# Kernel tuning notes

Measured on AMD Instinct MI355X. Metric: run time of the kernel, lower is better.

The kernel has to match this reference:

```python
import jax, jax.numpy as jnp
from jax import lax
import numpy as np

B, FRAMES, H, W = 8, 128, 64, 64
N_MFCC = 60
VID_FEAT = 196
D = VID_FEAT + N_MFCC   # COMBINE_SIZE = 256
ED = 2 * D              # mamba d_inner = 512
NST = 16                # d_state
DTR = 16                # dt_rank = ceil(D/16)
NL = 4                  # layers per direction
NC = 2                  # num_classes


def setup_inputs() -> dict:
    key = jax.random.key(0)
    ks = iter(jax.random.split(key, 64))
    def rn(shape, s=0.02):
        return jax.random.normal(next(ks), shape, jnp.float32) * s
    inp = {
        'video_input': jax.random.normal(next(ks), (B, FRAMES, 3, H, W), jnp.float32),
        'audio_input': jax.random.normal(next(ks), (B, FRAMES * N_MFCC), jnp.float32),
        'cnn_conv1_w': rn((32, 3, 3, 3), 0.1), 'cnn_conv1_b': jnp.zeros((32,), jnp.float32),
        'cnn_conv2_w': rn((64, 32, 3, 3), 0.05), 'cnn_conv2_b': jnp.zeros((64,), jnp.float32),
        'cnn_fc_w': rn((VID_FEAT, 64), 0.1), 'cnn_fc_b': jnp.zeros((VID_FEAT,), jnp.float32),
    }
    for pref in ('fwd', 'bwd'):
        inp[pref + '_norm_w'] = jnp.ones((NL, D), jnp.float32)
        inp[pref + '_in_proj_w'] = rn((NL, 2 * ED, D))
        inp[pref + '_conv_w'] = rn((NL, ED, 4), 0.1)
        inp[pref + '_conv_b'] = jnp.zeros((NL, ED), jnp.float32)
        inp[pref + '_x_proj_w'] = rn((NL, DTR + 2 * NST, ED))
        inp[pref + '_dt_w'] = rn((NL, ED, DTR), 0.1)
        inp[pref + '_dt_b'] = jnp.zeros((NL, ED), jnp.float32)
        inp[pref + '_A_log'] = jnp.tile(jnp.log(jnp.arange(1, NST + 1, dtype=jnp.float32)), (NL, ED, 1))
        inp[pref + '_D'] = jnp.ones((NL, ED), jnp.float32)
        inp[pref + '_out_proj_w'] = rn((NL, D, ED))
    inp['fc_w'] = rn((D, 2 * D)); inp['fc_b'] = jnp.zeros((D,), jnp.float32)
    inp['fc2_w'] = rn((NC, D)); inp['fc2_b'] = jnp.zeros((NC,), jnp.float32)
    return inp


def _rmsnorm(x, w, eps=1e-5):
    return x * lax.rsqrt(jnp.mean(x * x, -1, keepdims=True) + eps) * w


def _conv2d(x, w, b):
    y = lax.conv_general_dilated(x, w, (1, 1), 'SAME', dimension_numbers=('NCHW', 'OIHW', 'NCHW'))
    return y + b[None, :, None, None]


def _maxpool2(x):
    return lax.reduce_window(x, -jnp.inf, lax.max, (1, 1, 2, 2), (1, 1, 2, 2), 'VALID')


def _video_cnn(x, w1, b1, w2, b2, fw, fb):
    x = _maxpool2(jax.nn.relu(_conv2d(x, w1, b1)))
    x = _maxpool2(jax.nn.relu(_conv2d(x, w2, b2)))
    x = jnp.mean(x, (2, 3))            # global avg pool -> [B*F, 64]
    return x @ fw.T + fb               # [B*F, VID_FEAT]


def _mamba_layer(x, norm_w, in_w, conv_w, conv_b, xp_w, dt_w, dt_b, A_log, Dp, out_w):
    Bsz, L, _ = x.shape
    xn = _rmsnorm(x, norm_w)
    xz = jnp.einsum('bld,ed->ble', xn, in_w)        # [B,L,2*ED]
    xc, z = jnp.split(xz, 2, axis=-1)
    # causal depthwise conv1d, kernel 4
    xpad = jnp.pad(xc, ((0, 0), (3, 0), (0, 0)))
    xc = sum(xpad[:, k:k + L, :] * conv_w[:, k] for k in range(4)) + conv_b
    xc = jax.nn.silu(xc)
    dbc = jnp.einsum('ble,re->blr', xc, xp_w)       # [B,L,DTR+2*NST]
    dt, Bm, Cm = dbc[..., :DTR], dbc[..., DTR:DTR + NST], dbc[..., DTR + NST:]
    delta = jax.nn.softplus(jnp.einsum('blr,er->ble', dt, dt_w) + dt_b)  # [B,L,ED]
    A = -jnp.exp(A_log)                             # [ED,NST]
    dA = jnp.exp(delta[..., None] * A)              # [B,L,ED,NST]
    dBx = delta[..., None] * Bm[:, :, None, :] * xc[..., None]
    def step(h, inp):
        dA_t, dBx_t, c_t = inp
        h = dA_t * h + dBx_t
        return h, jnp.einsum('ben,bn->be', h, c_t)
    h0 = jnp.zeros((Bsz, ED, NST), x.dtype)
    _, ys = lax.scan(step, h0, (dA.transpose(1, 0, 2, 3), dBx.transpose(1, 0, 2, 3), Cm.transpose(1, 0, 2)))
    y = ys.transpose(1, 0, 2) + Dp * xc
    y = y * jax.nn.silu(z)
    return x + jnp.einsum('ble,de->bld', y, out_w)


def _mamba(x, norm_w, in_w, conv_w, conv_b, xp_w, dt_w, dt_b, A_log, Dp, out_w):
    for l in range(NL):
        x = _mamba_layer(x, norm_w[l], in_w[l], conv_w[l], conv_b[l], xp_w[l],
                         dt_w[l], dt_b[l], A_log[l], Dp[l], out_w[l])
    return x


def reference(video_input, audio_input, cnn_conv1_w, cnn_conv1_b, cnn_conv2_w, cnn_conv2_b,
              cnn_fc_w, cnn_fc_b,
              fwd_norm_w, fwd_in_proj_w, fwd_conv_w, fwd_conv_b, fwd_x_proj_w, fwd_dt_w,
              fwd_dt_b, fwd_A_log, fwd_D, fwd_out_proj_w,
              bwd_norm_w, bwd_in_proj_w, bwd_conv_w, bwd_conv_b, bwd_x_proj_w, bwd_dt_w,
              bwd_dt_b, bwd_A_log, bwd_D, bwd_out_proj_w,
              fc_w, fc_b, fc2_w, fc2_b):
    bsz, frames = video_input.shape[0], video_input.shape[1]
    xv = video_input.reshape(bsz * frames, 3, H, W)
    xv = _video_cnn(xv, cnn_conv1_w, cnn_conv1_b, cnn_conv2_w, cnn_conv2_b, cnn_fc_w, cnn_fc_b)
    xv = xv.reshape(bsz, frames, VID_FEAT)
    xa = audio_input.reshape(bsz, -1, N_MFCC)       # [B, frames, N_MFCC]
    xc = jnp.concatenate([xv, xa], axis=-1)         # [B, frames, D]
    xf = _mamba(xc, fwd_norm_w, fwd_in_proj_w, fwd_conv_w, fwd_conv_b, fwd_x_proj_w,
                fwd_dt_w, fwd_dt_b, fwd_A_log, fwd_D, fwd_out_proj_w)
    xb = _mamba(xc[:, ::-1], bwd_norm_w, bwd_in_proj_w, bwd_conv_w, bwd_conv_b, bwd_x_proj_w,
                bwd_dt_w, bwd_dt_b, bwd_A_log, bwd_D, bwd_out_proj_w)[:, ::-1]
    x_last = jnp.concatenate([xf, xb], axis=-1)[:, -1, :]   # [B, 2*D]; dropout = identity (eval)
    x = x_last @ fc_w.T + fc_b
    return x @ fc2_w.T + fc2_b
```

## Files before the change

kernel.cpp:

```cpp
#include <hip/hip_runtime.h>
#include <hip/hip_bf16.h>
#include <cstdint>
#include <cstddef>

#define BATCH 8
#define FRAMES 128
#define TOK (BATCH*FRAMES)
#define NM 60
#define VF 196
#define DD 256
#define EDIM 512
#define NSTATE 16
#define DTRANK 16
#define NLAYER 4

typedef __attribute__((ext_vector_type(8))) short short8v;
typedef __attribute__((ext_vector_type(4))) float f32x4;

__device__ __forceinline__ unsigned short f2bf(float f) {
  unsigned x = __float_as_uint(f);
  unsigned r = (x + 0x7FFFu + ((x >> 16) & 1u)) >> 16;
  return (unsigned short)r;
}

__global__ void pack_all(const float* __restrict__ ipF, const float* __restrict__ ipR,
                         const float* __restrict__ opF, const float* __restrict__ opR,
                         const float* __restrict__ xpF, const float* __restrict__ xpR,
                         const float* __restrict__ w2, const float* __restrict__ w1,
                         unsigned short* __restrict__ Wip, unsigned short* __restrict__ Wop,
                         unsigned short* __restrict__ Wxp, unsigned short* __restrict__ Wb,
                         unsigned short* __restrict__ Wb1) {
  int id = blockIdx.x * 256 + threadIdx.x;
  if (id < 262144) {
    int dl = id >> 15, r = id & 32767;
    int ntile = r >> 9, kt = (r >> 6) & 7, lane = r & 63;
    int dir = dl >> 2, layer = dl & 3;
    const float* src = (dir ? ipR : ipF) + (size_t)layer * 1024 * 256
                       + (size_t)(ntile * 16 + (lane & 15)) * 256 + kt * 32 + (lane >> 4) * 8;
    unsigned u[4];
#pragma unroll
    for (int p = 0; p < 4; ++p)
      u[p] = (unsigned)f2bf(src[2 * p]) | ((unsigned)f2bf(src[2 * p + 1]) << 16);
    uint4 v = {u[0], u[1], u[2], u[3]};
    *(uint4*)(Wip + (size_t)id * 8) = v;
  } else if (id < 262144 + 131072) {
    int id2 = id - 262144;
    int dl = id2 >> 14, rr = id2 & 16383;
    int ntile = rr >> 10, kt = (rr >> 6) & 15, lane = rr & 63;
    int dir = dl >> 2, layer = dl & 3;
    const float* src = (dir ? opR : opF) + (size_t)layer * 256 * 512
                       + (size_t)(ntile * 16 + (lane & 15)) * 512 + kt * 32 + (lane >> 4) * 8;
    unsigned u[4];
#pragma unroll
    for (int p = 0; p < 4; ++p)
      u[p] = (unsigned)f2bf(src[2 * p]) | ((unsigned)f2bf(src[2 * p + 1]) << 16);
    uint4 v = {u[0], u[1], u[2], u[3]};
    *(uint4*)(Wop + (size_t)id2 * 8) = v;
  } else if (id < 262144 + 131072 + 24576) {
    int id3 = id - 262144 - 131072;
    int dl = id3 / 3072, rr = id3 % 3072;
    int ntile = rr >> 10, kt = (rr >> 6) & 15, lane = rr & 63;
    int dir = dl >> 2, layer = dl & 3;
    const float* src = (dir ? xpR : xpF) + (size_t)layer * 48 * 512
                       + (size_t)(ntile * 16 + (lane & 15)) * 512 + kt * 32 + (lane >> 4) * 8;
    unsigned u[4];
#pragma unroll
    for (int p = 0; p < 4; ++p)
      u[p] = (unsigned)f2bf(src[2 * p]) | ((unsigned)f2bf(src[2 * p + 1]) << 16);
    uint4 v = {u[0], u[1], u[2], u[3]};
    *(uint4*)(Wxp + (size_t)id3 * 8) = v;
  } else if (id < 417792 + 2304) {
    int id4 = id - 417792;
    int lane = id4 & 63;
    int mt = (id4 >> 6) & 3;
    int sh = id4 >> 8;
    int dy = sh / 3, dx = sh % 3;
    int oc = mt * 16 + (lane & 15);
    int ic0 = (lane >> 4) * 8;
    unsigned u[4];
#pragma unroll
    for (int p = 0; p < 4; ++p) {
      unsigned short lo = f2bf(w2[((oc * 32 + ic0 + 2 * p) * 3 + dy) * 3 + dx]);
      unsigned short hi = f2bf(w2[((oc * 32 + ic0 + 2 * p + 1) * 3 + dy) * 3 + dx]);
      u[p] = (unsigned)lo | ((unsigned)hi << 16);
    }
    uint4 v = {u[0], u[1], u[2], u[3]};
    *(uint4*)(Wb + (size_t)id4 * 8) = v;
  } else if (id < 417792 + 2304 + 128) {
    int id5 = id - 417792 - 2304;
    int mt = id5 >> 6, lane = id5 & 63;
    int oc = mt * 16 + (lane & 15);
    int ko = lane >> 4;
    unsigned u[4];
#pragma unroll
    for (int p = 0; p < 4; ++p) {
      int k0 = ko * 8 + 2 * p, k1 = k0 + 1;
      unsigned short lo = (k0 < 27) ? f2bf(w1[oc * 27 + k0]) : 0;
      unsigned short hi = (k1 < 27) ? f2bf(w1[oc * 27 + k1]) : 0;
      u[p] = (unsigned)lo | ((unsigned)hi << 16);
    }
    uint4 v = {u[0], u[1], u[2], u[3]};
    *(uint4*)(Wb1 + (size_t)id5 * 8) = v;
  }
}

#define C1RS 68
#define C1ICS (66*68)
__global__ __launch_bounds__(256) void conv1_mfma(
    const float* __restrict__ video, const unsigned short* __restrict__ Wb1,
    const float* __restrict__ b1, unsigned short* __restrict__ X1)
{
  __shared__ unsigned short ldsu[3 * C1ICS + 96];
  const int img = blockIdx.x, t = threadIdx.x;
  const float* vin = video + (size_t)img * 12288;
  const int lane = t & 63, wv = t >> 6;
  const int col = lane & 15, ko = lane >> 4;

  for (int i = t; i < (3 * C1ICS + 96) / 2; i += 256) ((unsigned*)ldsu)[i] = 0;
  __syncthreads();
#pragma unroll
  for (int i = 0; i < 12; ++i) {
    int c = i * 256 + t;
    int ic = c >> 10, rem = c & 1023, gy = rem >> 4, c4 = rem & 15;
    float4 v = *(const float4*)(vin + ic * 4096 + gy * 64 + c4 * 4);
    unsigned lo = (unsigned)f2bf(v.x) | ((unsigned)f2bf(v.y) << 16);
    unsigned hi = (unsigned)f2bf(v.z) | ((unsigned)f2bf(v.w) << 16);
    int di = ic * C1ICS + (gy + 1) * C1RS + 4 + c4 * 4;
    *(uint2*)(ldsu + di) = (uint2){lo, hi};
  }

  short8v A0 = *(const short8v*)(Wb1 + (size_t)(0 * 64 + lane) * 8);
  short8v A1 = *(const short8v*)(Wb1 + (size_t)(1 * 64 + lane) * 8);
  float bia[2][4];
#pragma unroll
  for (int mt = 0; mt < 2; ++mt)
#pragma unroll
    for (int r = 0; r < 4; ++r) bia[mt][r] = b1[mt * 16 + ko * 4 + r];

  int offs[8];
#pragma unroll
  for (int j = 0; j < 8; ++j) {
    int k = ko * 8 + j;
    int o = 0;
    if (k < 27) {
      int ic = k / 9, tap = k - ic * 9;
      int dy = tap / 3, dx = tap - dy * 3;
      o = ic * C1ICS + dy * C1RS + dx + 3;
    }
    offs[j] = o;
  }
  __syncthreads();

  f32x4 z4 = {0.f, 0.f, 0.f, 0.f};
#pragma unroll 1
  for (int rp = 0; rp < 8; ++rp) {
    const int y0 = wv * 16 + rp * 2;
#pragma unroll
    for (int xg = 0; xg < 4; ++xg) {
      const int bse = y0 * C1RS + xg * 16 + col;
      short8v vb0, vb1;
#pragma unroll
      for (int j = 0; j < 8; ++j) {
        vb0[j] = (short)ldsu[bse + offs[j]];
        vb1[j] = (short)ldsu[bse + C1RS + offs[j]];
      }
      f32x4 c00 = __builtin_amdgcn_mfma_f32_16x16x32_bf16(A0, vb0, z4, 0, 0, 0);
      f32x4 c10 = __builtin_amdgcn_mfma_f32_16x16x32_bf16(A1, vb0, z4, 0, 0, 0);
      f32x4 c01 = __builtin_amdgcn_mfma_f32_16x16x32_bf16(A0, vb1, z4, 0, 0, 0);
      f32x4 c11 = __builtin_amdgcn_mfma_f32_16x16x32_bf16(A1, vb1, z4, 0, 0, 0);
      const int py = wv * 8 + rp;
      const int pxp = xg * 8 + (col >> 1);
#pragma unroll
      for (int mt = 0; mt < 2; ++mt) {
        f32x4 ca = mt ? c10 : c00;
        f32x4 cb = mt ? c11 : c01;
        unsigned pk[2];
#pragma unroll
        for (int r = 0; r < 4; ++r) {
          float va = fmaxf(ca[r] + bia[mt][r], 0.f);
          float vb = fmaxf(cb[r] + bia[mt][r], 0.f);
          float v = fmaxf(va, vb);
          v = fmaxf(v, __shfl_xor(v, 1, 64));
          unsigned short u = f2bf(v);
          if ((r & 1) == 0) pk[r >> 1] = (unsigned)u;
          else              pk[r >> 1] |= ((unsigned)u << 16);
        }
        if ((col & 1) == 0) {
          uint2 o = {pk[0], pk[1]};
          *(uint2*)(X1 + ((size_t)(img * 1024 + py * 32 + pxp) * 32 + mt * 16 + ko * 4)) = o;
        }
      }
    }
  }
}

#define OCT_STRIDE  (1156 * 16 + 32)
#define X_LDS_BYTES (4 * OCT_STRIDE)
__global__ __launch_bounds__(256) void conv2_k(
    const unsigned short* __restrict__ X1, const unsigned short* __restrict__ Wb,
    const float* __restrict__ b2, float* __restrict__ feat)
{
  extern __shared__ char sm[];
  float* part = (float*)(sm + X_LDS_BYTES);
  const int img = blockIdx.x, t = threadIdx.x;
  const int lane = t & 63, wv = t >> 6;
  const int kg = lane >> 4, l15 = lane & 15;

  for (int j = t; j < 1156; j += 256) {
    int r = j / 34, cc = j - r * 34;
    if (r == 0 || r == 33 || cc == 0 || cc == 33) {
      uint4 z = {0, 0, 0, 0};
#pragma unroll
      for (int oct = 0; oct < 4; ++oct)
        *(uint4*)(sm + oct * OCT_STRIDE + j * 16) = z;
    }
  }
  const uint4* src = (const uint4*)(X1 + (size_t)img * 32768);
#pragma unroll 4
  for (int i = 0; i < 16; ++i) {
    int c = i * 256 + t;
    uint4 v = src[c];
    int oct = c & 3, P = c >> 2;
    int y = P >> 5, x = P & 31;
    *(uint4*)(sm + oct * OCT_STRIDE + ((y + 1) * 34 + (x + 1)) * 16) = v;
  }
  __syncthreads();

  float bia[4][4];
#pragma unroll
  for (int mt = 0; mt < 4; ++mt)
#pragma unroll
    for (int r = 0; r < 4; ++r) bia[mt][r] = b2[mt * 16 + kg * 4 + r];

  float msum[4][4];
#pragma unroll
  for (int mt = 0; mt < 4; ++mt)
#pragma unroll
    for (int r = 0; r < 4; ++r) msum[mt][r] = 0.f;

#pragma unroll 1
  for (int pass = 0; pass < 2; ++pass) {
#pragma unroll 1
    for (int hf = 0; hf < 2; ++hf) {
      f32x4 acc[4][4];
#pragma unroll
      for (int mt = 0; mt < 4; ++mt)
#pragma unroll
        for (int q = 0; q < 4; ++q) acc[mt][q] = (f32x4){0.f, 0.f, 0.f, 0.f};
      int Pq[4];
#pragma unroll
      for (int q = 0; q < 4; ++q) {
        int p = (wv * 16 + pass * 8 + hf * 4 + q) * 16 + l15;
        int y = p >> 5, x = p & 31;
        Pq[q] = y * 34 + x;
      }
#pragma unroll
      for (int sh = 0; sh < 9; ++sh) {
        const int dy = sh / 3, dx = sh % 3;
        const int shoff = (dy * 34 + dx) * 16;
        short8v Af[4];
#pragma unroll
        for (int mt = 0; mt < 4; ++mt)
          Af[mt] = *(const short8v*)(Wb + ((size_t)(sh * 4 + mt) * 64 + lane) * 8);
#pragma unroll
        for (int q = 0; q < 4; ++q) {
          short8v Bf = *(const short8v*)(sm + kg * OCT_STRIDE + Pq[q] * 16 + shoff);
#pragma unroll
          for (int mt = 0; mt < 4; ++mt)
            acc[mt][q] = __builtin_amdgcn_mfma_f32_16x16x32_bf16(Af[mt], Bf, acc[mt][q], 0, 0, 0);
        }
      }
#pragma unroll
      for (int mt = 0; mt < 4; ++mt) {
#pragma unroll
        for (int pr = 0; pr < 2; ++pr) {
          int qa = pr, qb = pr + 2;
#pragma unroll
          for (int r = 0; r < 4; ++r) {
            float va = fmaxf(acc[mt][qa][r] + bia[mt][r], 0.f);
            float vb = fmaxf(acc[mt][qb][r] + bia[mt][r], 0.f);
            float v = fmaxf(va, vb);
            v = fmaxf(v, __shfl_xor(v, 1, 64));
            msum[mt][r] += v;
          }
        }
      }
    }
  }
#pragma unroll
  for (int mt = 0; mt < 4; ++mt)
#pragma unroll
    for (int r = 0; r < 4; ++r) {
      float v = msum[mt][r];
      v += __shfl_xor(v, 1, 64);
      v += __shfl_xor(v, 2, 64);
      v += __shfl_xor(v, 4, 64);
      v += __shfl_xor(v, 8, 64);
      if (l15 == 0) part[wv * 64 + mt * 16 + kg * 4 + r] = v * 0.5f;
    }
  __syncthreads();
  if (t < 64)
    feat[(size_t)img * 64 + t] =
        (part[t] + part[64 + t] + part[128 + t] + part[192 + t]) * (1.f / 256.f);
}

__global__ __launch_bounds__(256) void fcgemm_k(
    const float* __restrict__ A, const float* __restrict__ B,
    const float* __restrict__ bias, const float* __restrict__ audio,
    float* __restrict__ xf, float* __restrict__ xr)
{
  __shared__ float sA[16][68];
  __shared__ float sB[16][68];
  const int t = threadIdx.x;
  const int m0 = blockIdx.x * 64;
  const int n0 = blockIdx.y * 64;
  const int tx = t & 15, ty = t >> 4;
  const int lk = t & 15, lr = t >> 4;
  float acc[4][4] = {};
  for (int k0 = 0; k0 < 64; k0 += 16) {
#pragma unroll
    for (int rr = 0; rr < 4; ++rr) {
      int m = m0 + lr + rr * 16;
      sA[lk][lr + rr * 16] = A[(size_t)m * 64 + k0 + lk];
      int n = n0 + lr + rr * 16;
      sB[lk][lr + rr * 16] = (n < VF) ? B[(size_t)n * 64 + k0 + lk] : 0.f;
    }
    __syncthreads();
#pragma unroll
    for (int kk = 0; kk < 16; ++kk) {
      float a0 = sA[kk][ty*4+0], a1 = sA[kk][ty*4+1], a2 = sA[kk][ty*4+2], a3 = sA[kk][ty*4+3];
      float b0 = sB[kk][tx*4+0], b1 = sB[kk][tx*4+1], b2 = sB[kk][tx*4+2], b3 = sB[kk][tx*4+3];
      acc[0][0]=fmaf(a0,b0,acc[0][0]); acc[0][1]=fmaf(a0,b1,acc[0][1]); acc[0][2]=fmaf(a0,b2,acc[0][2]); acc[0][3]=fmaf(a0,b3,acc[0][3]);
      acc[1][0]=fmaf(a1,b0,acc[1][0]); acc[1][1]=fmaf(a1,b1,acc[1][1]); acc[1][2]=fmaf(a1,b2,acc[1][2]); acc[1][3]=fmaf(a1,b3,acc[1][3]);
      acc[2][0]=fmaf(a2,b0,acc[2][0]); acc[2][1]=fmaf(a2,b1,acc[2][1]); acc[2][2]=fmaf(a2,b2,acc[2][2]); acc[2][3]=fmaf(a2,b3,acc[2][3]);
      acc[3][0]=fmaf(a3,b0,acc[3][0]); acc[3][1]=fmaf(a3,b1,acc[3][1]); acc[3][2]=fmaf(a3,b2,acc[3][2]); acc[3][3]=fmaf(a3,b3,acc[3][3]);
    }
    __syncthreads();
  }
#pragma unroll
  for (int i = 0; i < 4; ++i) {
    int m = m0 + ty * 4 + i;
    int b = m >> 7, l = m & 127;
    int mr = (b << 7) + (127 - l);
#pragma unroll
    for (int j = 0; j < 4; ++j) {
      int n = n0 + tx * 4 + j;
      float v;
      if (n < VF)       v = acc[i][j] + bias[n];
      else              v = audio[(size_t)b * (FRAMES * NM) + l * NM + (n - VF)];
      xf[(size_t)m * DD + n] = v;
      xr[(size_t)mr * DD + n] = v;
    }
  }
}

__global__ __launch_bounds__(256) void inproj_mfma3(
    const float* __restrict__ xF, const float* __restrict__ xR,
    const float* __restrict__ nwF, const float* __restrict__ nwR,
    const unsigned short* __restrict__ Wip, int layer,
    float* __restrict__ xzF, float* __restrict__ xzR)
{
  const int dir = blockIdx.z;
  const float* x = dir ? xR : xF;
  const float* nw = dir ? nwR : nwF;
  float* xz = dir ? xzR : xzF;
  __shared__ unsigned short sa[32 * 16 * 8];
  const int t = threadIdx.x;
  const int tok0 = blockIdx.x * 16;
  {
    const int tk = t >> 4, l16 = t & 15;
    const float* row = x + (size_t)(tok0 + tk) * DD + l16 * 16;
    float v[16];
    float ss = 0.f;
#pragma unroll
    for (int i = 0; i < 4; ++i) {
      float4 f = ((const float4*)row)[i];
      v[4*i] = f.x; v[4*i+1] = f.y; v[4*i+2] = f.z; v[4*i+3] = f.w;
      ss += f.x*f.x + f.y*f.y + f.z*f.z + f.w*f.w;
    }
    ss += __shfl_xor(ss, 1, 16);
    ss += __shfl_xor(ss, 2, 16);
    ss += __shfl_xor(ss, 4, 16);
    ss += __shfl_xor(ss, 8, 16);
    float scale = rsqrtf(ss * (1.f / DD) + 1e-5f);
    const float* nwp = nw + l16 * 16;
#pragma unroll
    for (int hh = 0; hh < 2; ++hh) {
      unsigned ub[4];
#pragma unroll
      for (int p = 0; p < 4; ++p) {
        unsigned short lo = f2bf(v[hh*8 + 2*p]     * scale * nwp[hh*8 + 2*p]);
        unsigned short hi = f2bf(v[hh*8 + 2*p + 1] * scale * nwp[hh*8 + 2*p + 1]);
        ub[p] = (unsigned)lo | ((unsigned)hi << 16);
      }
      int k0 = l16 * 16 + hh * 8;
      int kt = k0 >> 5, oct = (k0 >> 3) & 3;
      uint4 w4 = {ub[0], ub[1], ub[2], ub[3]};
      *(uint4*)(sa + ((size_t)(kt * 4 + oct) * 16 + tk) * 8) = w4;
    }
  }
  __syncthreads();
  const int lane = t & 63, w = t >> 6;
  short8v af[8];
#pragma unroll
  for (int kt = 0; kt < 8; ++kt)
    af[kt] = *(const short8v*)(sa + ((size_t)(kt * 4 + (lane >> 4)) * 16 + (lane & 15)) * 8);
#pragma unroll
  for (int ns = 0; ns < 4; ++ns) {
    const int ntile = blockIdx.y * 16 + w * 4 + ns;
    const unsigned short* wb = Wip + (((size_t)(dir * 4 + layer) * 512 + ntile * 8) * 64 + lane) * 8;
    f32x4 acc = (f32x4){0.f, 0.f, 0.f, 0.f};
#pragma unroll
    for (int kt = 0; kt < 8; ++kt) {
      short8v bf = *(const short8v*)(wb + (size_t)kt * 64 * 8);
      acc = __builtin_amdgcn_mfma_f32_16x16x32_bf16(af[kt], bf, acc, 0, 0, 0);
    }
#pragma unroll
    for (int r = 0; r < 4; ++r)
      xz[(size_t)(tok0 + (lane >> 4) * 4 + r) * 1024 + ntile * 16 + (lane & 15)] = acc[r];
  }
}

__global__ __launch_bounds__(256) void xprojf_k(
    const float* __restrict__ xzF, const float* __restrict__ xzR,
    const float* __restrict__ cwF, const float* __restrict__ cwR,
    const float* __restrict__ cbF, const float* __restrict__ cbR,
    const unsigned short* __restrict__ Wxp, int layer,
    float* __restrict__ xcF, float* __restrict__ xcR,
    float* __restrict__ dbF, float* __restrict__ dbR)
{
  const int dir = blockIdx.z;
  const float* xz = dir ? xzR : xzF;
  const float* cw = dir ? cwR : cwF;
  const float* cb = dir ? cbR : cbF;
  float* xc = dir ? xcR : xcF;
  float* db = dir ? dbR : dbF;
  __shared__ unsigned short sa[64 * 16 * 8];
  const int t = threadIdx.x;
  const int tok0 = blockIdx.x * 16;

#pragma unroll
  for (int ii = 0; ii < 4; ++ii) {
    int idx = ii * 256 + t;
    int tk = idx >> 6, tok = tok0 + tk;
    int e0 = (idx & 63) << 3;
    int l = tok & 127;
    const float* col = xz + (size_t)tok * 1024 + e0;

    float v3[8] = {}, v2[8] = {}, v1[8] = {}, v0[8];
    if (l >= 3) { *(float4*)v3 = *(const float4*)(col - 3072); *(float4*)(v3+4) = *(const float4*)(col - 3068); }
    if (l >= 2) { *(float4*)v2 = *(const float4*)(col - 2048); *(float4*)(v2+4) = *(const float4*)(col - 2044); }
    if (l >= 1) { *(float4*)v1 = *(const float4*)(col - 1024); *(float4*)(v1+4) = *(const float4*)(col - 1020); }
    *(float4*)v0 = *(const float4*)col; *(float4*)(v0+4) = *(const float4*)(col + 4);

    float cbv[8];
    *(float4*)cbv = *(const float4*)(cb + e0); *(float4*)(cbv+4) = *(const float4*)(cb + e0 + 4);

    float res[8];
#pragma unroll
    for (int j = 0; j < 8; ++j) {
      float4 cv = ((const float4*)cw)[e0 + j];
      float a = cbv[j];
      a = fmaf(cv.x, v3[j], a);
      a = fmaf(cv.y, v2[j], a);
      a = fmaf(cv.z, v1[j], a);
      a = fmaf(cv.w, v0[j], a);
      res[j] = a / (1.f + __expf(-a));
    }
    float4 r0 = {res[0], res[1], res[2], res[3]};
    float4 r1 = {res[4], res[5], res[6], res[7]};
    float* xcp = xc + (size_t)tok * EDIM + e0;
    *(float4*)xcp = r0; *(float4*)(xcp + 4) = r1;

    unsigned ub[4];
#pragma unroll
    for (int p = 0; p < 4; ++p)
      ub[p] = (unsigned)f2bf(res[2*p]) | ((unsigned)f2bf(res[2*p+1]) << 16);
    int c = (e0 >> 3) * 16 + tk;
    c ^= (c >> 4) & 15;
    uint4 w4 = {ub[0], ub[1], ub[2], ub[3]};
    *(uint4*)(sa + (size_t)c * 8) = w4;
  }
  __syncthreads();

  const int w = t >> 6, lane = t & 63;
  if (w < 3) {
    const int nt = w;
    const unsigned short* wbase = Wxp + ((size_t)(dir * 4 + layer) * 3 * 16 * 64) * 8;
    f32x4 acc = (f32x4){0.f, 0.f, 0.f, 0.f};
#pragma unroll
    for (int kt = 0; kt < 16; ++kt) {
      int c = (kt * 4 + (lane >> 4)) * 16 + (lane & 15);
      c ^= (c >> 4) & 15;
      short8v af = *(const short8v*)(sa + (size_t)c * 8);
      short8v bf = *(const short8v*)(wbase + ((size_t)(nt * 16 + kt) * 64 + lane) * 8);
      acc = __builtin_amdgcn_mfma_f32_16x16x32_bf16(af, bf, acc, 0, 0, 0);
    }
#pragma unroll
    for (int r = 0; r < 4; ++r)
      db[(size_t)(tok0 + (lane >> 4) * 4 + r) * 48 + nt * 16 + (lane & 15)] = acc[r];
  }
}

__global__ __launch_bounds__(256) void scan4_k(
    const float* __restrict__ xzF, const float* __restrict__ xzR,
    const float* __restrict__ xcF, const float* __restrict__ xcR,
    const float* __restrict__ dbF, const float* __restrict__ dbR,
    const float* __restrict__ dwF, const float* __restrict__ dwR,
    const float* __restrict__ dtbF, const float* __restrict__ dtbR,
    const float* __restrict__ AlF, const float* __restrict__ AlR,
    const float* __restrict__ DpF, const float* __restrict__ DpR,
    unsigned short* __restrict__ yoF, unsigned short* __restrict__ yoR)
{
  const int dir = blockIdx.z;
  const float* xz = dir ? xzR : xzF;
  const float* xc = dir ? xcR : xcF;
  const float* db = dir ? dbR : dbF;
  const float* dw = dir ? dwR : dwF;
  const float* dtbv = dir ? dtbR : dtbF;
  const float* Al = dir ? AlR : AlF;
  const float* Dp = dir ? DpR : DpF;
  unsigned short* yo = dir ? yoR : yoF;

  __shared__ float sdb[FRAMES * 48];
  __shared__ float sxc[FRAMES * 16];
  __shared__ float sgz[FRAMES * 16];
  __shared__ float sdl[FRAMES * 16];
  const int b = blockIdx.x >> 5;
  const int e0 = (blockIdx.x & 31) << 4;
  const int t = threadIdx.x, g = t >> 4, n = t & 15;
  const int e = e0 + g;

  const float* dbp = db + (size_t)b * FRAMES * 48;
  for (int i = t; i < FRAMES * 48 / 4; i += 256)
    ((float4*)sdb)[i] = ((const float4*)dbp)[i];
  for (int i = t; i < FRAMES * 16; i += 256) {
    int l = i >> 4, c = i & 15;
    int ee = e0 + c;
    sxc[i] = xc[(size_t)(b * FRAMES + l) * EDIM + ee];
    float zz = xz[(size_t)(b * FRAMES + l) * 1024 + 512 + ee];
    sgz[i] = zz / (1.f + __expf(-zz));
    const float* d = db + (size_t)(b * FRAMES + l) * 48;
    const float* w = dw + (size_t)ee * 16;
    float a = dtbv[ee];
#pragma unroll
    for (int q = 0; q < 4; ++q) {
      float4 dv = *(const float4*)(d + 4 * q);
      float4 wv = *(const float4*)(w + 4 * q);
      a = fmaf(dv.x, wv.x, a); a = fmaf(dv.y, wv.y, a);
      a = fmaf(dv.z, wv.z, a); a = fmaf(dv.w, wv.w, a);
    }
    sdl[i] = (a > 20.f) ? a : __logf(1.f + __expf(a));
  }
  float An = -expf(Al[e * NSTATE + n]);
  float Dv = Dp[e];
  float h = 0.f;
  unsigned short* yp = yo + ((size_t)((e >> 5) * 4 + ((e >> 3) & 3)) * 1024 + b * FRAMES) * 8 + (e & 7);
  __syncthreads();

#pragma unroll 1
  for (int l = 0; l < FRAMES; ++l) {
    float dlt = sdl[l * 16 + g];
    float xcv = sxc[l * 16 + g];
    float Bn = sdb[l * 48 + 16 + n];
    float Cn = sdb[l * 48 + 32 + n];
    float dA = __expf(dlt * An);
    h = fmaf(dA, h, dlt * xcv * Bn);
    float part = h * Cn;
    part += __shfl_xor(part, 1, 16);
    part += __shfl_xor(part, 2, 16);
    part += __shfl_xor(part, 4, 16);
    part += __shfl_xor(part, 8, 16);
    if (n == 0) {
      float a2 = fmaf(Dv, xcv, part);
      yp[(size_t)l * 8] = f2bf(a2 * sgz[l * 16 + g]);
    }
  }
}

__global__ __launch_bounds__(256) void outproj_mfma(
    const unsigned short* __restrict__ yoF, const unsigned short* __restrict__ yoR,
    const unsigned short* __restrict__ Wop, int layer,
    float* __restrict__ xF, float* __restrict__ xR)
{
  const int dir = blockIdx.z;
  const unsigned short* yo = dir ? yoR : yoF;
  float* xx = dir ? xR : xF;
  const int t = threadIdx.x, lane = t & 63, w = t >> 6;
  const int m0 = blockIdx.x * 32, n0 = blockIdx.y * 64;
  const int ntile = blockIdx.y * 4 + w;
  const unsigned short* wb = Wop + (((size_t)(dir * 4 + layer) * 256 + ntile * 16) * 64 + lane) * 8;
  f32x4 acc[2];
  acc[0] = (f32x4){0.f, 0.f, 0.f, 0.f};
  acc[1] = (f32x4){0.f, 0.f, 0.f, 0.f};
#pragma unroll
  for (int kt = 0; kt < 16; ++kt) {
    short8v bf = *(const short8v*)(wb + (size_t)kt * 64 * 8);
#pragma unroll
    for (int mt = 0; mt < 2; ++mt) {
      short8v af = *(const short8v*)(yo + ((size_t)(kt * 4 + (lane >> 4)) * 1024 + m0 + mt * 16 + (lane & 15)) * 8);
      acc[mt] = __builtin_amdgcn_mfma_f32_16x16x32_bf16(af, bf, acc[mt], 0, 0, 0);
    }
  }
#pragma unroll
  for (int mt = 0; mt < 2; ++mt)
#pragma unroll
    for (int r = 0; r < 4; ++r) {
      size_t ci = (size_t)(m0 + mt * 16 + (lane >> 4) * 4 + r) * DD + n0 + w * 16 + (lane & 15);
      xx[ci] += acc[mt][r];
    }
}

__global__ __launch_bounds__(256) void head_k(
    const float* __restrict__ xf, const float* __restrict__ xr,
    const float* __restrict__ fcw, const float* __restrict__ fcb,
    const float* __restrict__ fc2w, const float* __restrict__ fc2b,
    float* __restrict__ out)
{
  int b = blockIdx.x;
  __shared__ float xl[2 * DD];
  __shared__ float h[DD];
  __shared__ float hp[4];
  int t = threadIdx.x;
  xl[t]      = xf[(size_t)(b * FRAMES + FRAMES - 1) * DD + t];
  xl[DD + t] = xr[(size_t)(b * FRAMES + 0) * DD + t];
  __syncthreads();
  float acc = fcb[t];
  for (int k = 0; k < 2 * DD; ++k) acc = fmaf(xl[k], fcw[(size_t)t * 2 * DD + k], acc);
  h[t] = acc;
  __syncthreads();
  {
    int c = t >> 7, k = t & 127;
    float p = h[k] * fc2w[c * DD + k] + h[k + 128] * fc2w[c * DD + k + 128];
#pragma unroll
    for (int off = 32; off; off >>= 1) p += __shfl_xor(p, off, 64);
    if ((t & 63) == 0) hp[t >> 6] = p;
  }
  __syncthreads();
  if (t < 2) out[b * 2 + t] = hp[2 * t] + hp[2 * t + 1] + fc2b[t];
}

extern "C" void kernel_launch(void* const* d_in, const int* in_sizes, int n_in,
                              void* d_out, int out_size, void* d_ws, size_t ws_size,
                              hipStream_t stream) {
  const float* video = (const float*)d_in[0];
  const float* audio = (const float*)d_in[1];
  const float* c1w = (const float*)d_in[2];
  const float* c1b = (const float*)d_in[3];
  const float* c2w = (const float*)d_in[4];
  const float* c2b = (const float*)d_in[5];
  const float* fcw = (const float*)d_in[6];
  const float* fcb = (const float*)d_in[7];
  const float* Wf[10]; const float* Wb_[10];
  for (int i = 0; i < 10; ++i) { Wf[i] = (const float*)d_in[8+i]; Wb_[i] = (const float*)d_in[18+i]; }
  const float* fc_w  = (const float*)d_in[28];
  const float* fc_b  = (const float*)d_in[29];
  const float* fc2_w = (const float*)d_in[30];
  const float* fc2_b = (const float*)d_in[31];
  float* out = (float*)d_out;

  float* ws   = (float*)d_ws;
  float* feat = ws;
  float* xf   = feat + 65536;
  float* xr   = xf   + 262144;
  float* xzF  = xr   + 262144;
  float* xzR  = xzF  + 1048576;
  float* xcF  = xzR  + 1048576;
  float* xcR  = xcF  + 524288;
  float* dbF  = xcR  + 524288;
  float* dbR  = dbF  + 49152;
  unsigned short* yoF = (unsigned short*)(dbR + 49152);
  unsigned short* yoR = yoF + 524288;
  unsigned short* X1  = yoR + 524288;
  unsigned short* Wbp = X1 + 33554432;
  unsigned short* Wip = Wbp + 18432;
  unsigned short* Wop = Wip + 2097152;
  unsigned short* Wxp = Wop + 1048576;
  unsigned short* Wb1 = Wxp + 196608;

  pack_all<<<dim3(1642), 256, 0, stream>>>(Wf[1], Wb_[1], Wf[9], Wb_[9], Wf[4], Wb_[4],
                                           c2w, c1w, Wip, Wop, Wxp, Wbp, Wb1);
  conv1_mfma<<<dim3(TOK), 256, 0, stream>>>(video, Wb1, c1b, X1);
  conv2_k<<<dim3(TOK), 256, (size_t)(X_LDS_BYTES + 1024), stream>>>(X1, Wbp, c2b, feat);

  fcgemm_k<<<dim3(16, 4), 256, 0, stream>>>(feat, fcw, fcb, audio, xf, xr);

  for (int l = 0; l < NLAYER; ++l) {
    const float* nwF  = Wf[0] + l*DD;              const float* nwR  = Wb_[0] + l*DD;
    const float* cwF_ = Wf[2] + l*EDIM*4;          const float* cwR_ = Wb_[2] + l*EDIM*4;
    const float* cbF_ = Wf[3] + l*EDIM;            const float* cbR_ = Wb_[3] + l*EDIM;
    const float* dwF  = Wf[5] + l*EDIM*DTRANK;     const float* dwR  = Wb_[5] + l*EDIM*DTRANK;
    const float* dtbF = Wf[6] + l*EDIM;            const float* dtbR = Wb_[6] + l*EDIM;
    const float* AlF  = Wf[7] + l*EDIM*NSTATE;     const float* AlR  = Wb_[7] + l*EDIM*NSTATE;
    const float* DpF  = Wf[8] + l*EDIM;            const float* DpR  = Wb_[8] + l*EDIM;

    inproj_mfma3<<<dim3(64, 4, 2), 256, 0, stream>>>(xf, xr, nwF, nwR, Wip, l, xzF, xzR);
    xprojf_k<<<dim3(64, 1, 2), 256, 0, stream>>>(xzF, xzR, cwF_, cwR_, cbF_, cbR_,
                                                 Wxp, l, xcF, xcR, dbF, dbR);
    scan4_k<<<dim3(256, 1, 2), 256, 0, stream>>>(xzF, xzR, xcF, xcR, dbF, dbR, dwF, dwR,
                                                 dtbF, dtbR, AlF, AlR, DpF, DpR, yoF, yoR);
    outproj_mfma<<<dim3(32, 4, 2), 256, 0, stream>>>(yoF, yoR, Wop, l, xf, xr);
  }

  head_k<<<dim3(BATCH), 256, 0, stream>>>(xf, xr, fc_w, fc_b, fc2_w, fc2_b, out);
}
```

Baseline: 362.5 us.

## Store in_proj output as bf16 and split conv2 accumulation into two passes

The in_proj activations (xz) are now written as bf16 instead of fp32, and the conv and scan kernels that read them are changed to match. This halves the memory traffic for that intermediate. The conv2 inner loop is also split into two sub-passes of two pixel quads each, which halves the accumulator registers per pass and should improve occupancy, at the cost of reloading the weight fragments twice. Rounding xz to bf16 adds some error to the Mamba layers.

```diff
diff --git a/kernel.cpp b/kernel.cpp
--- a/kernel.cpp
+++ b/kernel.cpp
@@ -21,6 +21,9 @@
   unsigned x = __float_as_uint(f);
   unsigned r = (x + 0x7FFFu + ((x >> 16) & 1u)) >> 16;
   return (unsigned short)r;
+}
+__device__ __forceinline__ float bf2f(unsigned short u) {
+  return __uint_as_float((unsigned)u << 16);
 }
 
 __global__ void pack_all(const float* __restrict__ ipF, const float* __restrict__ ipR,
@@ -242,48 +245,48 @@
   for (int pass = 0; pass < 2; ++pass) {
 #pragma unroll 1
     for (int hf = 0; hf < 2; ++hf) {
-      f32x4 acc[4][4];
-#pragma unroll
-      for (int mt = 0; mt < 4; ++mt)
-#pragma unroll
-        for (int q = 0; q < 4; ++q) acc[mt][q] = (f32x4){0.f, 0.f, 0.f, 0.f};
-      int Pq[4];
-#pragma unroll
-      for (int q = 0; q < 4; ++q) {
-        int p = (wv * 16 + pass * 8 + hf * 4 + q) * 16 + l15;
-        int y = p >> 5, x = p & 31;
-        Pq[q] = y * 34 + x;
-      }
-#pragma unroll
-      for (int sh = 0; sh < 9; ++sh) {
-        const int dy = sh / 3, dx = sh % 3;
-        const int shoff = (dy * 34 + dx) * 16;
-        short8v Af[4];
+#pragma unroll 1
+      for (int qq = 0; qq < 2; ++qq) {
+        f32x4 acc[4][2];
+#pragma unroll
+        for (int mt = 0; mt < 4; ++mt) {
+          acc[mt][0] = (f32x4){0.f, 0.f, 0.f, 0.f};
+          acc[mt][1] = (f32x4){0.f, 0.f, 0.f, 0.f};
+        }
+        int Pq[2];
+#pragma unroll
+        for (int j = 0; j < 2; ++j) {
+          int qsel = qq + j * 2;
+          int p = (wv * 16 + pass * 8 + hf * 4 + qsel) * 16 + l15;
+          int y = p >> 5, x = p & 31;
+          Pq[j] = y * 34 + x;
+        }
+#pragma unroll
+        for (int sh = 0; sh < 9; ++sh) {
+          const int dy = sh / 3, dx = sh % 3;
+          const int shoff = (dy * 34 + dx) * 16;
+          short8v Af[4];
+#pragma unroll
+          for (int mt = 0; mt < 4; ++mt)
+            Af[mt] = *(const short8v*)(Wb + ((size_t)(sh * 4 + mt) * 64 + lane) * 8);
+          short8v B0 = *(const short8v*)(sm + kg * OCT_STRIDE + Pq[0] * 16 + shoff);
+          short8v B1 = *(const short8v*)(sm + kg * OCT_STRIDE + Pq[1] * 16 + shoff);
+#pragma unroll
+          for (int mt = 0; mt < 4; ++mt) {
+            acc[mt][0] = __builtin_amdgcn_mfma_f32_16x16x32_bf16(Af[mt], B0, acc[mt][0], 0, 0, 0);
+            acc[mt][1] = __builtin_amdgcn_mfma_f32_16x16x32_bf16(Af[mt], B1, acc[mt][1], 0, 0, 0);
+          }
+        }
 #pragma unroll
         for (int mt = 0; mt < 4; ++mt)
-          Af[mt] = *(const short8v*)(Wb + ((size_t)(sh * 4 + mt) * 64 + lane) * 8);
-#pragma unroll
-        for (int q = 0; q < 4; ++q) {
-          short8v Bf = *(const short8v*)(sm + kg * OCT_STRIDE + Pq[q] * 16 + shoff);
-#pragma unroll
-          for (int mt = 0; mt < 4; ++mt)
-            acc[mt][q] = __builtin_amdgcn_mfma_f32_16x16x32_bf16(Af[mt], Bf, acc[mt][q], 0, 0, 0);
-        }
-      }
-#pragma unroll
-      for (int mt = 0; mt < 4; ++mt) {
-#pragma unroll
-        for (int pr = 0; pr < 2; ++pr) {
-          int qa = pr, qb = pr + 2;
 #pragma unroll
           for (int r = 0; r < 4; ++r) {
-            float va = fmaxf(acc[mt][qa][r] + bia[mt][r], 0.f);
-            float vb = fmaxf(acc[mt][qb][r] + bia[mt][r], 0.f);
+            float va = fmaxf(acc[mt][0][r] + bia[mt][r], 0.f);
+            float vb = fmaxf(acc[mt][1][r] + bia[mt][r], 0.f);
             float v = fmaxf(va, vb);
             v = fmaxf(v, __shfl_xor(v, 1, 64));
             msum[mt][r] += v;
           }
-        }
       }
     }
   }
@@ -358,12 +361,12 @@
     const float* __restrict__ xF, const float* __restrict__ xR,
     const float* __restrict__ nwF, const float* __restrict__ nwR,
     const unsigned short* __restrict__ Wip, int layer,
-    float* __restrict__ xzF, float* __restrict__ xzR)
+    unsigned short* __restrict__ xzF, unsigned short* __restrict__ xzR)
 {
   const int dir = blockIdx.z;
   const float* x = dir ? xR : xF;
   const float* nw = dir ? nwR : nwF;
-  float* xz = dir ? xzR : xzF;
+  unsigned short* xz = dir ? xzR : xzF;
   __shared__ unsigned short sa[32 * 16 * 8];
   const int t = threadIdx.x;
   const int tok0 = blockIdx.x * 16;
@@ -417,12 +420,12 @@
     }
 #pragma unroll
     for (int r = 0; r < 4; ++r)
-      xz[(size_t)(tok0 + (lane >> 4) * 4 + r) * 1024 + ntile * 16 + (lane & 15)] = acc[r];
+      xz[(size_t)(tok0 + (lane >> 4) * 4 + r) * 1024 + ntile * 16 + (lane & 15)] = f2bf(acc[r]);
   }
 }
 
 __global__ __launch_bounds__(256) void xprojf_k(
-    const float* __restrict__ xzF, const float* __restrict__ xzR,
+    const unsigned short* __restrict__ xzF, const unsigned short* __restrict__ xzR,
     const float* __restrict__ cwF, const float* __restrict__ cwR,
     const float* __restrict__ cbF, const float* __restrict__ cbR,
     const unsigned short* __restrict__ Wxp, int layer,
@@ -430,7 +433,7 @@
     float* __restrict__ dbF, float* __restrict__ dbR)
 {
   const int dir = blockIdx.z;
-  const float* xz = dir ? xzR : xzF;
+  const unsigned short* xz = dir ? xzR : xzF;
   const float* cw = dir ? cwR : cwF;
   const float* cb = dir ? cbR : cbF;
   float* xc = dir ? xcR : xcF;
@@ -445,13 +448,13 @@
     int tk = idx >> 6, tok = tok0 + tk;
     int e0 = (idx & 63) << 3;
     int l = tok & 127;
-    const float* col = xz + (size_t)tok * 1024 + e0;
-
-    float v3[8] = {}, v2[8] = {}, v1[8] = {}, v0[8];
-    if (l >= 3) { *(float4*)v3 = *(const float4*)(col - 3072); *(float4*)(v3+4) = *(const float4*)(col - 3068); }
-    if (l >= 2) { *(float4*)v2 = *(const float4*)(col - 2048); *(float4*)(v2+4) = *(const float4*)(col - 2044); }
-    if (l >= 1) { *(float4*)v1 = *(const float4*)(col - 1024); *(float4*)(v1+4) = *(const float4*)(col - 1020); }
-    *(float4*)v0 = *(const float4*)col; *(float4*)(v0+4) = *(const float4*)(col + 4);
+    const unsigned short* col = xz + (size_t)tok * 1024 + e0;
+
+    unsigned short v3[8] = {}, v2[8] = {}, v1[8] = {}, v0[8];
+    if (l >= 3) *(uint4*)v3 = *(const uint4*)(col - 3 * 1024);
+    if (l >= 2) *(uint4*)v2 = *(const uint4*)(col - 2 * 1024);
+    if (l >= 1) *(uint4*)v1 = *(const uint4*)(col - 1 * 1024);
+    *(uint4*)v0 = *(const uint4*)col;
 
     float cbv[8];
     *(float4*)cbv = *(const float4*)(cb + e0); *(float4*)(cbv+4) = *(const float4*)(cb + e0 + 4);
@@ -461,10 +464,10 @@
     for (int j = 0; j < 8; ++j) {
       float4 cv = ((const float4*)cw)[e0 + j];
       float a = cbv[j];
-      a = fmaf(cv.x, v3[j], a);
-      a = fmaf(cv.y, v2[j], a);
-      a = fmaf(cv.z, v1[j], a);
-      a = fmaf(cv.w, v0[j], a);
+      a = fmaf(cv.x, bf2f(v3[j]), a);
+      a = fmaf(cv.y, bf2f(v2[j]), a);
+      a = fmaf(cv.z, bf2f(v1[j]), a);
+      a = fmaf(cv.w, bf2f(v0[j]), a);
       res[j] = a / (1.f + __expf(-a));
     }
     float4 r0 = {res[0], res[1], res[2], res[3]};
@@ -503,7 +506,7 @@
 }
 
 __global__ __launch_bounds__(256) void scan4_k(
-    const float* __restrict__ xzF, const float* __restrict__ xzR,
+    const unsigned short* __restrict__ xzF, const unsigned short* __restrict__ xzR,
     const float* __restrict__ xcF, const float* __restrict__ xcR,
     const float* __restrict__ dbF, const float* __restrict__ dbR,
     const float* __restrict__ dwF, const float* __restrict__ dwR,
@@ -513,7 +516,7 @@
     unsigned short* __restrict__ yoF, unsigned short* __restrict__ yoR)
 {
   const int dir = blockIdx.z;
-  const float* xz = dir ? xzR : xzF;
+  const unsigned short* xz = dir ? xzR : xzF;
   const float* xc = dir ? xcR : xcF;
   const float* db = dir ? dbR : dbF;
   const float* dw = dir ? dwR : dwF;
@@ -538,7 +541,7 @@
     int l = i >> 4, c = i & 15;
     int ee = e0 + c;
     sxc[i] = xc[(size_t)(b * FRAMES + l) * EDIM + ee];
-    float zz = xz[(size_t)(b * FRAMES + l) * 1024 + 512 + ee];
+    float zz = bf2f(xz[(size_t)(b * FRAMES + l) * 1024 + 512 + ee]);
     sgz[i] = zz / (1.f + __expf(-zz));
     const float* d = db + (size_t)(b * FRAMES + l) * 48;
     const float* w = dw + (size_t)ee * 16;
@@ -663,9 +666,9 @@
   float* feat = ws;
   float* xf   = feat + 65536;
   float* xr   = xf   + 262144;
-  float* xzF  = xr   + 262144;
-  float* xzR  = xzF  + 1048576;
-  float* xcF  = xzR  + 1048576;
+  unsigned short* xzF = (unsigned short*)(xr + 262144);
+  unsigned short* xzR = (unsigned short*)(xr + 262144 + 1048576);
+  float* xcF  = xr + 262144 + 2097152;
   float* xcR  = xcF  + 524288;
   float* dbF  = xcR  + 524288;
   float* dbR  = dbF  + 49152;
```

After: 349.4 us. -3.6%, faster.
